# Kernel tuning notes

Measured on AMD Instinct MI355X. Metric: run time of the kernel, lower is better.

The kernel has to match this reference:

```python
import jax, jax.numpy as jnp
import numpy as np

C = 128          # channels (d_model)
D_STATE = 16
D_CONV = 4
EXPAND = 2
D_INNER = EXPAND * C       # 256
DT_RANK = (C + 15) // 16   # 8 (ceil(d_model/16))
B_SZ, H, W = 4, 64, 64


def setup_inputs() -> dict:
    key = jax.random.key(0)
    ks = jax.random.split(key, 12)
    n = lambda k, s, sc=0.02: jax.random.normal(k, s, dtype=jnp.float32) * sc
    return {
        "x": jax.random.normal(ks[0], (B_SZ, C, H, W), dtype=jnp.float32),
        # spatial 3x3 conv
        "conv_spatial_w": n(ks[1], (C, C, 3, 3)),
        "conv_spatial_b": jnp.zeros((C,), jnp.float32),
        # spectral 1x1 conv on [real; imag] concat (2C -> 2C)
        "conv_spectral_w": n(ks[2], (2 * C, 2 * C, 1, 1)),
        "conv_spectral_b": jnp.zeros((2 * C,), jnp.float32),
        # Mamba params (mamba_ssm defaults: in/out_proj no bias, conv1d+dt_proj bias)
        "in_proj_w": n(ks[3], (2 * D_INNER, C)),
        "conv1d_w": n(ks[4], (D_INNER, 1, D_CONV), 0.2),  # depthwise, groups=d_inner
        "conv1d_b": jnp.zeros((D_INNER,), jnp.float32),
        "x_proj_w": n(ks[5], (DT_RANK + 2 * D_STATE, D_INNER)),
        "dt_proj_w": n(ks[6], (D_INNER, DT_RANK), 0.1),
        "dt_proj_b": n(ks[7], (D_INNER,), 0.1),
        "A_log": jnp.log(jnp.broadcast_to(jnp.arange(1, D_STATE + 1, dtype=jnp.float32), (D_INNER, D_STATE))),
        "D": jnp.ones((D_INNER,), jnp.float32),
        "out_proj_w": n(ks[8], (C, D_INNER)),
    }


def _selective_scan(x, dt, A, B, Cm, D):
    # x, dt: [b,l,d]; B, Cm: [b,l,n]; A: [d,n]; D: [d]
    b, l, d = x.shape

    def step(h, inp):
        xt, dtt, Bt, Ct = inp  # [b,d],[b,d],[b,n],[b,n]
        dA = jnp.exp(dtt[..., None] * A)                     # [b,d,n]
        h = dA * h + dtt[..., None] * Bt[:, None, :] * xt[..., None]
        y = jnp.einsum('bdn,bn->bd', h, Ct)
        return h, y

    h0 = jnp.zeros((b, d, A.shape[1]), x.dtype)
    xs = (x.transpose(1, 0, 2), dt.transpose(1, 0, 2),
          B.transpose(1, 0, 2), Cm.transpose(1, 0, 2))
    _, ys = jax.lax.scan(step, h0, xs)
    return ys.transpose(1, 0, 2) + x * D                     # skip term D*x


def _mamba(u, in_proj_w, conv1d_w, conv1d_b, x_proj_w, dt_proj_w, dt_proj_b, A_log, D, out_proj_w):
    # u: [b, l, d_model]
    xz = jnp.einsum('bld,ed->ble', u, in_proj_w)             # [b,l,2*d_inner]
    xi, z = jnp.split(xz, 2, axis=-1)
    # causal depthwise conv1d over sequence
    xc = jax.lax.conv_general_dilated(
        xi.transpose(0, 2, 1), conv1d_w, (1,), ((D_CONV - 1, 0),),
        dimension_numbers=('NCH', 'OIH', 'NCH'), feature_group_count=D_INNER)
    xs = jax.nn.silu((xc + conv1d_b[None, :, None]).transpose(0, 2, 1))  # [b,l,d_inner]
    x_dbl = jnp.einsum('bld,rd->blr', xs, x_proj_w)
    dt = jax.nn.softplus(
        jnp.einsum('blr,dr->bld', x_dbl[..., :DT_RANK], dt_proj_w) + dt_proj_b)
    Bm = x_dbl[..., DT_RANK:DT_RANK + D_STATE]
    Cm = x_dbl[..., DT_RANK + D_STATE:]
    A = -jnp.exp(A_log)
    y = _selective_scan(xs, dt, A, Bm, Cm, D)
    y = y * jax.nn.silu(z)
    return jnp.einsum('bld,od->blo', y, out_proj_w)


def reference(x, conv_spatial_w, conv_spatial_b, conv_spectral_w, conv_spectral_b,
              in_proj_w, conv1d_w, conv1d_b, x_proj_w, dt_proj_w, dt_proj_b,
              A_log, D, out_proj_w):
    b, c, h, w = x.shape
    # spatial branch: 3x3 conv, padding 1
    spatial = jax.lax.conv_general_dilated(
        x, conv_spatial_w, (1, 1), ((1, 1), (1, 1)),
        dimension_numbers=('NCHW', 'OIHW', 'NCHW')) + conv_spatial_b[None, :, None, None]
    # mamba branch over flattened spatial sequence
    u = x.transpose(0, 2, 3, 1).reshape(b, h * w, c)
    ym = _mamba(u, in_proj_w, conv1d_w, conv1d_b, x_proj_w, dt_proj_w, dt_proj_b,
                A_log, D, out_proj_w)
    ym = ym.reshape(b, h, w, c).transpose(0, 3, 1, 2)
    # spectral branch: rfft2 -> concat(real,imag) -> 1x1 conv -> complex -> irfft2
    fft = jnp.fft.rfft2(x, axes=(-2, -1))                    # [b,c,h,w//2+1]
    cat = jnp.concatenate([fft.real, fft.imag], axis=1)      # [b,2c,h,w//2+1]
    fc = jnp.einsum('bchw,oc->bohw', cat, conv_spectral_w[:, :, 0, 0]) \
         + conv_spectral_b[None, :, None, None]
    fr, fi = jnp.split(fc, 2, axis=1)
    spectral = jnp.fft.irfft2(jax.lax.complex(fr, fi), s=(h, w), axes=(-2, -1))
    return spatial + spectral + ym
```

## Files before the change

kernel.cpp:

```cpp
#include <hip/hip_runtime.h>
#include <math.h>

#define PI2 6.283185307179586f
#define SPEC_P 2112
#define NC 64
#define LC 64

typedef __attribute__((ext_vector_type(8))) short s8v;
typedef __attribute__((ext_vector_type(4))) float f4v;
typedef __attribute__((ext_vector_type(4))) unsigned int u4v;
typedef __attribute__((ext_vector_type(4))) unsigned short u16x4;

__device__ __forceinline__ float sigmoidf_(float v){ return 1.0f/(1.0f+__expf(-v)); }
__device__ __forceinline__ float siluf_(float v){ return v*sigmoidf_(v); }
__device__ __forceinline__ float softplusf_(float v){ return fmaxf(v,0.0f)+log1pf(__expf(-fabsf(v))); }
__device__ __forceinline__ float bf2f(ushort u){ union{unsigned u; float f;} x; x.u=((unsigned)u)<<16; return x.f; }
__device__ __forceinline__ ushort f2bf(float f){ union{float f; unsigned u;} x; x.f=f; return (ushort)((x.u + 0x7FFFu + ((x.u>>16)&1u))>>16); }
__device__ __forceinline__ float u2f_hi(unsigned w){ union{unsigned u; float f;} x; x.u = w & 0xffff0000u; return x.f; }
__device__ __forceinline__ float u2f_lo(unsigned w){ union{unsigned u; float f;} x; x.u = w << 16; return x.f; }

__global__ void __launch_bounds__(256) k_prep_all(
        const float* __restrict__ x, const float* __restrict__ csw,
        const float* __restrict__ dtw, const float* __restrict__ xpw,
        const float* __restrict__ ipw, const float* __restrict__ opw,
        const float* __restrict__ spw, const float* __restrict__ c1w,
        ushort* __restrict__ xT, ushort* __restrict__ wsp, ushort* __restrict__ cxw,
        ushort* __restrict__ ipwb, ushort* __restrict__ opwb, ushort* __restrict__ spwb,
        ushort* __restrict__ gE1, ushort* __restrict__ gE2f,
        ushort* __restrict__ gE2i, ushort* __restrict__ gE3,
        float* __restrict__ cwT){
    __shared__ float ld[128][65];
    int tid=threadIdx.x;
    if(blockIdx.x < 256){
        int bh=blockIdx.x; int b=bh>>6, h=bh&63;
        for(int i=tid;i<8192;i+=256){ int c=i>>6, w=i&63;
            ld[c][w] = x[((size_t)((b<<7)+c)<<12) + (h<<6) + w]; }
        __syncthreads();
        for(int i=tid;i<8192;i+=256){ int w=i>>7, c=i&127;
            xT[((size_t)bh<<13) + (w<<7) + c] = f2bf(ld[c][w]); }
        return;
    }
    int i = (blockIdx.x-256)*256+tid;
    if(i<147456){
        int p = i>>14; int rem = i&16383; int o=rem>>7, c=rem&127;
        wsp[i] = f2bf(csw[(size_t)(o*128+c)*9 + p]);
    } else if(i<212992){
        int j = i-147456; int e=j>>8, c=j&255;
        float s=0.f;
        #pragma unroll
        for(int r=0;r<8;r++) s += dtw[e*8+r]*xpw[r*256+c];
        cxw[j]=f2bf(s);
    } else if(i<221184){
        int t=i-212992; cxw[65536+t]=f2bf(xpw[2048+t]);
    } else if(i<286720){
        int t=i-221184; ipwb[t]=f2bf(ipw[t]);
    } else if(i<319488){
        int t=i-286720; opwb[t]=f2bf(opw[t]);
    } else if(i<385024){
        int t=i-319488; spwb[t]=f2bf(spw[t]);
    } else if(i<389248){
        int j=i-385024; int r=j>>6, w=j&63; float v;
        if(r<33){ int t=(w*r)&63; v = cosf(PI2*(float)t/64.0f); }
        else    { int t=(w*(r-33))&63; v = -sinf(PI2*(float)t/64.0f); }
        gE1[j]=f2bf(v);
    } else if(i<405632){
        int j=i-389248; int col=j>>7, k=j&127; int h=k&63, rk=k>>6, kh=col&63, rc=col>>6;
        int t=(h*kh)&63; float cv=cosf(PI2*(float)t/64.0f), sv=sinf(PI2*(float)t/64.0f);
        float v = (rc==0) ? (rk==0? cv : sv) : (rk==0? -sv : cv);
        gE2f[j]=f2bf(v);
    } else if(i<422016){
        int j=i-405632; int col=j>>7, k=j&127; int h=col&63, rc=col>>6, kh=k&63, rk=k>>6;
        int t=(h*kh)&63; float cv=cosf(PI2*(float)t/64.0f), sv=sinf(PI2*(float)t/64.0f);
        float v = (rc==0) ? (rk==0? cv : -sv) : (rk==0? sv : cv);
        gE2i[j]=f2bf(v);
    } else if(i<428160){
        int j=i-422016; int w=j/96, k=j-w*96; float v=0.f;
        if(k<33){
            int kw=k;
            if(kw==0) v=1.f;
            else if(kw==32) v=(w&1)? -1.f : 1.f;
            else { int t=(kw*w)&63; v=2.f*cosf(PI2*(float)t/64.0f); }
        } else if(k<66){
            int kw=k-33;
            if(kw==0||kw==32) v=0.f;
            else { int t=(kw*w)&63; v=-2.f*sinf(PI2*(float)t/64.0f); }
        }
        gE3[j]=f2bf(v);
    } else if(i<429184){
        int j=i-428160; int k=j>>8, d=j&255;
        cwT[j] = c1w[d*4+k];
    }
}

template<int BM,int BN,int WR,int WC,int BK,int KT>
__device__ __forceinline__ void gemm_body(const ushort* __restrict__ Ag, int lda,
                                          const ushort* __restrict__ Bg, int ldb,
                                          int m0, int n0, f4v* acc, ushort* smem){
    constexpr int MR = BM/(WR*16);
    constexpr int NR = BN/(WC*16);
    constexpr int AW = BK+8;
    ushort (*As)[AW] = (ushort(*)[AW])smem;
    ushort (*Bs)[AW] = (ushort(*)[AW])(smem + BM*AW);
    const int tid=threadIdx.x, lane=tid&63, wid=tid>>6;
    const int l15=lane&15, lhi=lane>>4;
    const int wr=wid/WC, wc=wid%WC;
    for(int kb=0;kb<KT;kb++){
        __syncthreads();
        for(int v=tid; v<BM*(BK/8); v+=256){ int r=v/(BK/8), cv=(v%(BK/8))*8;
            *(s8v*)&As[r][cv] = *(const s8v*)&Ag[(size_t)(m0+r)*lda + kb*BK + cv]; }
        for(int v=tid; v<BN*(BK/8); v+=256){ int r=v/(BK/8), cv=(v%(BK/8))*8;
            *(s8v*)&Bs[r][cv] = *(const s8v*)&Bg[(size_t)(n0+r)*ldb + kb*BK + cv]; }
        __syncthreads();
        #pragma unroll
        for(int ck=0;ck<BK/32;ck++){
            s8v a[MR], bb[NR];
            #pragma unroll
            for(int i=0;i<MR;i++) a[i] = *(const s8v*)&As[wr*(BM/WR)+i*16+l15][ck*32+lhi*8];
            #pragma unroll
            for(int j=0;j<NR;j++) bb[j] = *(const s8v*)&Bs[wc*(BN/WC)+j*16+l15][ck*32+lhi*8];
            #pragma unroll
            for(int i=0;i<MR;i++)
                #pragma unroll
                for(int j=0;j<NR;j++)
                    acc[i*NR+j] = __builtin_amdgcn_mfma_f32_16x16x32_bf16(a[i], bb[j], acc[i*NR+j],0,0,0);
        }
    }
}

__device__ __forceinline__ void body_spatial(int bx, const ushort* __restrict__ xT,
        const ushort* __restrict__ wsp, const float* __restrict__ csb,
        float* __restrict__ out, ushort* smem){
    ushort (*slab)[66][72] = (ushort(*)[66][72])smem;
    int bh = bx>>1, oh = bx&1;
    int b = bh>>6, h = bh&63;
    int tid = threadIdx.x, lane = tid&63, wid = tid>>6;
    int l15 = lane&15, lhi = lane>>4;
    s8v zv = {0,0,0,0,0,0,0,0};
    if(tid < 48){
        int khp = tid>>4; int rem = tid&15;
        int row = (rem>>3)*65, cv = (rem&7)*8;
        *(s8v*)&slab[khp][row][cv] = zv;
    }
    f4v acc[4];
    f4v zf = {0.f,0.f,0.f,0.f};
    #pragma unroll
    for(int j=0;j<4;j++) acc[j]=zf;
    int orow = oh*64 + wid*16 + l15;
    for(int kb=0;kb<2;kb++){
        __syncthreads();
        for(int khh=0;khh<3;khh++){
            int hh = h-1+khh;
            if(hh>=0 && hh<64){
                const ushort* src = xT + (((size_t)(b<<6)+hh)<<13) + kb*64;
                for(int v=tid; v<512; v+=256){
                    int w = v>>3, cv = (v&7)*8;
                    *(s8v*)&slab[khh][w+1][cv] = *(const s8v*)&src[(w<<7)+cv];
                }
            } else {
                for(int v=tid; v<512; v+=256){
                    int w = v>>3, cv = (v&7)*8;
                    *(s8v*)&slab[khh][w+1][cv] = zv;
                }
            }
        }
        __syncthreads();
        for(int p=0;p<9;p++){
            int khh = p/3, kw = p - khh*3;
            const ushort* wrow = wsp + (size_t)p*16384 + (orow<<7) + kb*64;
            #pragma unroll
            for(int ck=0;ck<2;ck++){
                s8v a = *(const s8v*)&wrow[ck*32+lhi*8];
                #pragma unroll
                for(int j=0;j<4;j++){
                    s8v bf = *(const s8v*)&slab[khh][j*16+l15+kw][ck*32+lhi*8];
                    acc[j] = __builtin_amdgcn_mfma_f32_16x16x32_bf16(a, bf, acc[j],0,0,0);
                }
            }
        }
    }
    #pragma unroll
    for(int r=0;r<4;r++){
        int o = oh*64 + wid*16 + lhi*4 + r;
        float bv = csb[o];
        size_t rowbase = (((size_t)(b<<7)+o)<<12) + (h<<6);
        #pragma unroll
        for(int j=0;j<4;j++){
            out[rowbase + j*16 + l15] = acc[j][r] + bv;
        }
    }
}

__device__ __forceinline__ void body_inproj(int j, const ushort* __restrict__ xT,
        const ushort* __restrict__ ipw, ushort* __restrict__ xi, ushort* __restrict__ z,
        ushort* smem){
    int m0 = (j&127)*128, n0 = (j>>7)*128;
    f4v acc[16];
    f4v zf = {0.f,0.f,0.f,0.f};
    #pragma unroll
    for(int q=0;q<16;q++) acc[q]=zf;
    gemm_body<128,128,2,2,64,2>(xT,128, ipw,128, m0,n0, acc, smem);
    int tid=threadIdx.x, lane=tid&63, wid=tid>>6, l15=lane&15, lhi=lane>>4;
    int wr=wid>>1, wc=wid&1;
    #pragma unroll
    for(int i=0;i<4;i++)
        #pragma unroll
        for(int jj=0;jj<4;jj++)
            #pragma unroll
            for(int r=0;r<4;r++){
                int m = m0 + wr*64 + i*16 + lhi*4 + r;
                int e = n0 + wc*64 + jj*16 + l15;
                ushort v = f2bf(acc[i*4+jj][r]);
                if(e<256) xi[(size_t)m*256+e]=v; else z[(size_t)m*256+e-256]=v;
            }
}

__device__ __forceinline__ void body_spec_fwd(int bc, const float* __restrict__ x,
        const ushort* __restrict__ gE1, const ushort* __restrict__ gE2f,
        ushort* __restrict__ rit, ushort* smem){
    ushort (*Xs)[72]  = (ushort(*)[72])smem;
    ushort (*E1s)[72] = (ushort(*)[72])(smem+4608);
    ushort (*T2s)[136]= (ushort(*)[136])(smem+10368);
    ushort (*EB)[72]  = (ushort(*)[72])smem;
    int b = bc>>7, c = bc&127;
    int tid=threadIdx.x, lane=tid&63, wid=tid>>6, l15=lane&15, lhi=lane>>4;
    const float* xsrc = x + ((size_t)bc<<12);
    for(int v=tid; v<1024; v+=256){
        int h=v>>4, w0=(v&15)<<2;
        float4 f = *(const float4*)&xsrc[(h<<6)+w0];
        Xs[h][w0]=f2bf(f.x); Xs[h][w0+1]=f2bf(f.y); Xs[h][w0+2]=f2bf(f.z); Xs[h][w0+3]=f2bf(f.w);
    }
    for(int v=tid; v<528; v+=256){ int r=v>>3, k0=(v&7)<<3;
        *(s8v*)&E1s[r][k0] = *(const s8v*)&gE1[(r<<6)+k0]; }
    __syncthreads();
    {
        f4v accA[5];
        f4v zf={0.f,0.f,0.f,0.f};
        #pragma unroll
        for(int j=0;j<5;j++) accA[j]=zf;
        int m0 = wid<<4;
        #pragma unroll
        for(int ck=0;ck<2;ck++){
            s8v a = *(const s8v*)&Xs[m0+l15][ck*32+lhi*8];
            #pragma unroll
            for(int j=0;j<5;j++){
                s8v bb = *(const s8v*)&E1s[j*16+l15][ck*32+lhi*8];
                accA[j] = __builtin_amdgcn_mfma_f32_16x16x32_bf16(a, bb, accA[j],0,0,0);
            }
        }
        #pragma unroll
        for(int j=0;j<5;j++){
            int c_ = j*16+l15;
            #pragma unroll
            for(int r=0;r<4;r++){
                int h = m0 + lhi*4 + r;
                if(c_ < 33)      T2s[c_][h]       = f2bf(accA[j][r]);
                else if(c_ < 66) T2s[c_-33][64+h] = f2bf(accA[j][r]);
            }
        }
    }
    f4v accB[6];
    {
        f4v zf={0.f,0.f,0.f,0.f};
        #pragma unroll
        for(int q=0;q<6;q++) accB[q]=zf;
    }
    for(int kb=0;kb<2;kb++){
        __syncthreads();
        for(int v=tid; v<1024; v+=256){ int r=v>>3, k0=(v&7)<<3;
            *(s8v*)&EB[r][k0] = *(const s8v*)&gE2f[(r<<7) + kb*64 + k0]; }
        __syncthreads();
        #pragma unroll
        for(int rt=0; rt<3; rt++){
            #pragma unroll
            for(int ck=0;ck<2;ck++){
                s8v a  = *(const s8v*)&T2s[rt*16+l15][kb*64 + ck*32+lhi*8];
                s8v b0 = *(const s8v*)&EB[(wid*2)*16+l15][ck*32+lhi*8];
                s8v b1 = *(const s8v*)&EB[(wid*2+1)*16+l15][ck*32+lhi*8];
                accB[rt*2+0] = __builtin_amdgcn_mfma_f32_16x16x32_bf16(a, b0, accB[rt*2+0],0,0,0);
                accB[rt*2+1] = __builtin_amdgcn_mfma_f32_16x16x32_bf16(a, b1, accB[rt*2+1],0,0,0);
            }
        }
    }
    #pragma unroll
    for(int rt=0; rt<3; rt++){
        int col0 = wid*32 + l15;
        int col1 = wid*32 + 16 + l15;
        int kh0 = col0&63, ri0 = col0>>6;
        int kh1 = col1&63, ri1 = col1>>6;
        #pragma unroll
        for(int r=0;r<4;r++){
            int kw = rt*16 + lhi*4 + r;
            if(kw<33){
                rit[((size_t)(b*2112) + kh0*33 + kw)*256 + ri0*128 + c] = f2bf(accB[rt*2+0][r]);
                rit[((size_t)(b*2112) + kh1*33 + kw)*256 + ri1*128 + c] = f2bf(accB[rt*2+1][r]);
            }
        }
    }
}

__global__ void __launch_bounds__(256) k_stage1(
        const float* __restrict__ x, const ushort* __restrict__ xT,
        const ushort* __restrict__ wsp, const float* __restrict__ csb,
        const ushort* __restrict__ ipwb, const ushort* __restrict__ gE1,
        const ushort* __restrict__ gE2f,
        float* __restrict__ out, ushort* __restrict__ xi, ushort* __restrict__ zb,
        ushort* __restrict__ rit){
    __shared__ __align__(16) ushort smem[18432];
    int bx = blockIdx.x;
    if(bx < 512)       body_spatial(bx, xT, wsp, csb, out, smem);
    else if(bx < 1024) body_inproj(bx-512, xT, ipwb, xi, zb, smem);
    else               body_spec_fwd(bx-1024, x, gE1, gE2f, rit, smem);
}

__device__ __forceinline__ void body_conv1d(int blk, const ushort* __restrict__ xi,
        const float* __restrict__ cwT, const float* __restrict__ cb, ushort* __restrict__ xs){
    int flat = blk*256 + threadIdx.x;
    int d8 = (flat & 31) << 3;
    int bl = flat >> 5;
    int l  = bl & 4095;
    s8v zv = {0,0,0,0,0,0,0,0};
    s8v x0 = *(const s8v*)&xi[(size_t)bl*256 + d8];
    s8v x1 = (l>=1)? *(const s8v*)&xi[(size_t)(bl-1)*256 + d8] : zv;
    s8v x2 = (l>=2)? *(const s8v*)&xi[(size_t)(bl-2)*256 + d8] : zv;
    s8v x3 = (l>=3)? *(const s8v*)&xi[(size_t)(bl-3)*256 + d8] : zv;
    f4v w0a = *(const f4v*)&cwT[0*256+d8], w0b = *(const f4v*)&cwT[0*256+d8+4];
    f4v w1a = *(const f4v*)&cwT[1*256+d8], w1b = *(const f4v*)&cwT[1*256+d8+4];
    f4v w2a = *(const f4v*)&cwT[2*256+d8], w2b = *(const f4v*)&cwT[2*256+d8+4];
    f4v w3a = *(const f4v*)&cwT[3*256+d8], w3b = *(const f4v*)&cwT[3*256+d8+4];
    f4v ba  = *(const f4v*)&cb[d8], bbv = *(const f4v*)&cb[d8+4];
    s8v outv;
    #pragma unroll
    for(int j=0;j<8;j++){
        float w0 = (j<4)? w0a[j] : w0b[j-4];
        float w1 = (j<4)? w1a[j] : w1b[j-4];
        float w2 = (j<4)? w2a[j] : w2b[j-4];
        float w3 = (j<4)? w3a[j] : w3b[j-4];
        float bs = (j<4)? ba[j]  : bbv[j-4];
        float acc = bs + bf2f((ushort)x3[j])*w0 + bf2f((ushort)x2[j])*w1
                       + bf2f((ushort)x1[j])*w2 + bf2f((ushort)x0[j])*w3;
        outv[j] = (short)f2bf(siluf_(acc));
    }
    *(s8v*)&xs[(size_t)bl*256 + d8] = outv;
}

__global__ void __launch_bounds__(256) k_stage2(
        const ushort* __restrict__ xi, const float* __restrict__ cwT,
        const float* __restrict__ c1b, ushort* __restrict__ xs,
        const ushort* __restrict__ rit, const ushort* __restrict__ spwb,
        const float* __restrict__ spb, ushort* __restrict__ Frb, ushort* __restrict__ Fib){
    __shared__ __align__(16) ushort smem[13824];
    int bx = blockIdx.x;
    if(bx < 2048){ body_conv1d(bx, xi, cwT, c1b, xs); return; }
    int jj = bx - 2048;
    int nt = jj/132, mt = jj - nt*132;
    int m0 = mt*64, n0 = nt*128;
    f4v acc[8];
    f4v zf = {0.f,0.f,0.f,0.f};
    #pragma unroll
    for(int q=0;q<8;q++) acc[q]=zf;
    gemm_body<64,128,2,2,64,4>(rit,256, spwb,256, m0,n0, acc, smem);
    int tid=threadIdx.x, lane=tid&63, wid=tid>>6, l15=lane&15, lhi=lane>>4;
    int wr=wid>>1, wc=wid&1;
    #pragma unroll
    for(int i=0;i<2;i++)
        #pragma unroll
        for(int j=0;j<4;j++){
            int m = m0 + wr*32 + i*16 + lhi*4;
            int bb = m/SPEC_P, p = m - bb*SPEC_P;
            int e = n0 + wc*64 + j*16 + l15;
            f4v v = acc[i*4+j] + spb[e];
            u16x4 pk;
            pk.x=f2bf(v[0]); pk.y=f2bf(v[1]); pk.z=f2bf(v[2]); pk.w=f2bf(v[3]);
            ushort* dst = (e<128)? &Frb[((size_t)(bb*128+e))*SPEC_P+p]
                                 : &Fib[((size_t)(bb*128+e-128))*SPEC_P+p];
            *(u16x4*)dst = pk;
        }
}

__device__ __forceinline__ void body_xdbl(int j, const ushort* __restrict__ xs,
        const ushort* __restrict__ cxw, const float* __restrict__ dtb,
        ushort* __restrict__ dtBC, ushort* smem){
    int m0 = (j&127)*128, n0 = (j>>7)*96;
    f4v acc[12];
    f4v zf = {0.f,0.f,0.f,0.f};
    #pragma unroll
    for(int q=0;q<12;q++) acc[q]=zf;
// ... 24 lines not shown
    const ushort* fr = Frb + (size_t)bo*SPEC_P;
    const ushort* fi = Fib + (size_t)bo*SPEC_P;
    for(int p=tid; p<2112; p+=256){
        int kh = p/33, kw = p - kh*33;
        A1s[kw][kh]    = fr[p];
        A1s[kw][64+kh] = fi[p];
    }
    f4v accB[6];
    {
        f4v zf={0.f,0.f,0.f,0.f};
        #pragma unroll
        for(int q=0;q<6;q++) accB[q]=zf;
    }
    for(int kb=0;kb<2;kb++){
        __syncthreads();
        for(int v=tid; v<1024; v+=256){ int r=v>>3, k0=(v&7)<<3;
            *(s8v*)&EB[r][k0] = *(const s8v*)&gE2i[(r<<7) + kb*64 + k0]; }
        __syncthreads();
        #pragma unroll
        for(int rt=0; rt<3; rt++){
            #pragma unroll
            for(int ck=0;ck<2;ck++){
                s8v a  = *(const s8v*)&A1s[rt*16+l15][kb*64 + ck*32+lhi*8];
                s8v b0 = *(const s8v*)&EB[(wid*2)*16+l15][ck*32+lhi*8];
                s8v b1 = *(const s8v*)&EB[(wid*2+1)*16+l15][ck*32+lhi*8];
                accB[rt*2+0] = __builtin_amdgcn_mfma_f32_16x16x32_bf16(a, b0, accB[rt*2+0],0,0,0);
                accB[rt*2+1] = __builtin_amdgcn_mfma_f32_16x16x32_bf16(a, b1, accB[rt*2+1],0,0,0);
            }
        }
    }
    __syncthreads();
    {
        s8v zvv = {0,0,0,0,0,0,0,0};
        for(int v=tid; v<256; v+=256){}
        if(tid<256){ int r=tid>>2, c0=64+((tid&3)<<3); *(s8v*)&T3s[r][c0]=zvv; }
    }
    for(int v=tid; v<768; v+=256){ int r=v/12, k0=(v-r*12)*8;
        *(s8v*)&E3s[r][k0] = *(const s8v*)&gE3[r*96+k0]; }
    __syncthreads();
    #pragma unroll
    for(int rt=0; rt<3; rt++){
        int col0 = wid*32 + l15;
        int col1 = wid*32 + 16 + l15;
        int h0 = col0&63, ri0 = col0>>6;
        int h1 = col1&63, ri1 = col1>>6;
        #pragma unroll
        for(int r=0;r<4;r++){
            int kw = rt*16 + lhi*4 + r;
            if(kw<33){
                T3s[h0][ri0? 33+kw : kw] = f2bf(accB[rt*2+0][r]);
                T3s[h1][ri1? 33+kw : kw] = f2bf(accB[rt*2+1][r]);
            }
        }
    }
    __syncthreads();
    {
        int m0 = wid<<4;
        f4v acc[4];
        f4v zf={0.f,0.f,0.f,0.f};
        #pragma unroll
        for(int j=0;j<4;j++) acc[j]=zf;
        #pragma unroll
        for(int ck=0;ck<3;ck++){
            s8v a = *(const s8v*)&T3s[m0+l15][ck*32+lhi*8];
            #pragma unroll
            for(int j=0;j<4;j++){
                s8v bb = *(const s8v*)&E3s[j*16+l15][ck*32+lhi*8];
                acc[j] = __builtin_amdgcn_mfma_f32_16x16x32_bf16(a, bb, acc[j],0,0,0);
            }
        }
        ushort* obase = specT + ((size_t)bo<<12);
        #pragma unroll
        for(int j=0;j<4;j++){
            int w = j*16+l15;
            #pragma unroll
            for(int r=0;r<4;r++){
                int h = m0 + lhi*4 + r;
                obase[(h<<6)+w] = f2bf(acc[j][r]*(1.0f/4096.0f));
            }
        }
    }
}

__global__ void __launch_bounds__(256) k_stage3(
        const ushort* __restrict__ xs, const ushort* __restrict__ cxw,
        const float* __restrict__ dtb, ushort* __restrict__ dtBC,
        const ushort* __restrict__ Frb, const ushort* __restrict__ Fib,
        const ushort* __restrict__ gE2i, const ushort* __restrict__ gE3,
        ushort* __restrict__ specT){
    __shared__ __align__(16) ushort smem[16128];
    int bx = blockIdx.x;
    if(bx < 384) body_xdbl(bx, xs, cxw, dtb, dtBC, smem);
    else         body_spec_inv(bx-384, Frb, Fib, gE2i, gE3, specT, smem);
}

__global__ void __launch_bounds__(256) k_scan(
        const ushort* __restrict__ xs, const ushort* __restrict__ dtBC,
        const ushort* __restrict__ z, const float* __restrict__ A_log,
        const float* __restrict__ Dp, ushort* __restrict__ ys){
    __shared__ unsigned sdx[LC*16];
    __shared__ unsigned sbc[LC*16];
    __shared__ ushort   sz[LC*16];
    __shared__ float    sY[16*272];
    int blk = blockIdx.x;
    int c   = blk & (NC-1);
    int bdg = blk >> 6;
    int b = bdg >> 4, dg = bdg & 15;
    int d_base = dg*16;
    int tid = threadIdx.x;
    int g = tid>>4, n = tid&15;
    int d = d_base + g;
    float An = -__expf(A_log[d*16+n]);
    float DdR = Dp[d_base + n];
    {
        int lc = tid>>2, part = tid&3;
        size_t r = (size_t)(b*4096 + c*64 + lc);
        if(part<2){
// ... 32 lines not shown
    for(int t4=0;t4<4;t4++){
        #pragma unroll
        for(int k=0;k<16;k++){
            int lc = t4*16+k;
            unsigned wdx = pdx[lc*16];
            unsigned wbc = pbc[lc*16];
            float dtv = u2f_lo(wdx);
            float xv  = u2f_hi(wdx);
            float Bv  = u2f_lo(wbc);
            float Cv  = u2f_hi(wbc);
            float dA  = __expf(dtv*An);
            h = dA*h + (dtv*xv)*Bv;
            psy[k*272] = h*Cv;
        }
        __syncthreads();
        {
            float s = 0.f;
            const float* pr = &sY[tt*272 + g2];
            #pragma unroll
            for(int n2=0;n2<16;n2++) s += pr[n2*17];
            int lcg = t4*16+tt;
            float xv2 = u2f_hi(sdx[lcg*16+g2]);
            float zv  = bf2f(sz[lcg*16+g2]);
            float yv  = (s + xv2*DdR) * siluf_(zv);
            ys[(size_t)(b*4096 + c*64 + lcg)*256 + d_base + g2] = f2bf(yv);
        }
        __syncthreads();
    }
}

__global__ void __launch_bounds__(256) k_final(const ushort* __restrict__ ys,
                                               const ushort* __restrict__ opw,
                                               const ushort* __restrict__ specT,
                                               float* __restrict__ out){
    __shared__ __align__(16) ushort smem[13824];
    int m0 = blockIdx.x*64;
    f4v acc[8];
    f4v zf = {0.f,0.f,0.f,0.f};
    #pragma unroll
    for(int q=0;q<8;q++) acc[q]=zf;
    gemm_body<64,128,2,2,64,4>(ys,256, opw,256, m0,0, acc, smem);
    int tid=threadIdx.x, lane=tid&63, wid=tid>>6, l15=lane&15, lhi=lane>>4;
    int wr=wid>>1, wc=wid&1;
    #pragma unroll
    for(int i=0;i<2;i++)
        #pragma unroll
        for(int j=0;j<4;j++){
            int m = m0 + wr*32 + i*16 + lhi*4;
            int o = wc*64 + j*16 + l15;
            int bb = m>>12, l = m&4095;
            size_t oidx = (((size_t)(bb<<7)+o)<<12)+l;
            f4v old = *(f4v*)&out[oidx];
            u16x4 sp = *(const u16x4*)&specT[oidx];
            f4v spv = {bf2f(sp.x), bf2f(sp.y), bf2f(sp.z), bf2f(sp.w)};
            *(f4v*)&out[oidx] = old + acc[i*4+j] + spv;
        }
}

extern "C" void kernel_launch(void* const* d_in, const int* in_sizes, int n_in,
                              void* d_out, int out_size, void* d_ws, size_t ws_size,
                              hipStream_t stream){
    const float* x    = (const float*)d_in[0];
    const float* csw  = (const float*)d_in[1];
    const float* csb  = (const float*)d_in[2];
    const float* spw  = (const float*)d_in[3];
    const float* spb  = (const float*)d_in[4];
    const float* ipw  = (const float*)d_in[5];
    const float* c1w  = (const float*)d_in[6];
    const float* c1b  = (const float*)d_in[7];
    const float* xpw  = (const float*)d_in[8];
    const float* dtw  = (const float*)d_in[9];
    const float* dtb  = (const float*)d_in[10];
    const float* alog = (const float*)d_in[11];
    const float* Dp   = (const float*)d_in[12];
    const float* opw  = (const float*)d_in[13];
    float* out = (float*)d_out;

    ushort* uw   = (ushort*)d_ws;
    ushort* xT   = uw;
    ushort* wsp  = xT + 2097152;
    ushort* ipwb = wsp + 147456;
    ushort* cxw  = ipwb + 65536;
    ushort* opwb = cxw + 73728;
    ushort* spwb = opwb + 32768;
    ushort* gE1  = spwb + 65536;
    ushort* gE2f = gE1 + 4352;
    ushort* gE2i = gE2f + 16384;
    ushort* gE3  = gE2i + 16384;
    ushort* xi   = gE3 + 6144;
    ushort* zb   = xi + 4194304;
    ushort* xs   = zb + 4194304;
    ushort* dtBC = xs + 4194304;
    ushort* Frb  = dtBC + 4718592;
    ushort* Fib  = Frb + 2162688;
    ushort* rit  = Fib + 2162688;
    float*  cwT  = (float*)(rit + 2162688);
    ushort* specT = rit;

    k_prep_all<<<1933,256,0,stream>>>(x, csw, dtw, xpw, ipw, opw, spw, c1w,
                                      xT, wsp, cxw, ipwb, opwb, spwb,
                                      gE1, gE2f, gE2i, gE3, cwT);
    k_stage1<<<1536,256,0,stream>>>(x, xT, wsp, csb, ipwb, gE1, gE2f,
                                    out, xi, zb, rit);
    k_stage2<<<2312,256,0,stream>>>(xi, cwT, c1b, xs, rit, spwb, spb, Frb, Fib);
    k_stage3<<<896,256,0,stream>>>(xs, cxw, dtb, dtBC, Frb, Fib, gE2i, gE3, specT);
    k_scan<<<4096,256,0,stream>>>(xs, dtBC, zb, alog, Dp, xi );
    k_final<<<256,256,0,stream>>>(xi , opwb, specT, out);
}
```

Baseline: 136.4 us.

## Restructure pipeline: fuse conv1d into in-proj, move spectral forward into prep kernel

The spectral forward DFT now runs inside the first (prep) kernel, with twiddles generated in shared memory rather than loaded from global tables. The in-projection is split into an x-half that applies the causal depthwise conv1d and SiLU in its epilogue using a 16-row halo, and a separate z-half. That removes the standalone conv1d pass and the round trip of xi through memory. The spatial conv output goes to a bf16 buffer summed in the final kernel, so the read-modify-write of out is gone at some precision cost. The final GEMM tile is halved to launch more blocks, and the halo rows recompute extra in-projection work.

Measured after the change: 141.3 us. +3.6%, slower.

```diff
diff --git a/kernel.cpp b/kernel.cpp
--- a/kernel.cpp
+++ b/kernel.cpp
@@ -18,79 +18,6 @@
 __device__ __forceinline__ ushort f2bf(float f){ union{float f; unsigned u;} x; x.f=f; return (ushort)((x.u + 0x7FFFu + ((x.u>>16)&1u))>>16); }
 __device__ __forceinline__ float u2f_hi(unsigned w){ union{unsigned u; float f;} x; x.u = w & 0xffff0000u; return x.f; }
 __device__ __forceinline__ float u2f_lo(unsigned w){ union{unsigned u; float f;} x; x.u = w << 16; return x.f; }
-
-__global__ void __launch_bounds__(256) k_prep_all(
-        const float* __restrict__ x, const float* __restrict__ csw,
-        const float* __restrict__ dtw, const float* __restrict__ xpw,
-        const float* __restrict__ ipw, const float* __restrict__ opw,
-        const float* __restrict__ spw, const float* __restrict__ c1w,
-        ushort* __restrict__ xT, ushort* __restrict__ wsp, ushort* __restrict__ cxw,
-        ushort* __restrict__ ipwb, ushort* __restrict__ opwb, ushort* __restrict__ spwb,
-        ushort* __restrict__ gE1, ushort* __restrict__ gE2f,
-        ushort* __restrict__ gE2i, ushort* __restrict__ gE3,
-        float* __restrict__ cwT){
-    __shared__ float ld[128][65];
-    int tid=threadIdx.x;
-    if(blockIdx.x < 256){
-        int bh=blockIdx.x; int b=bh>>6, h=bh&63;
-        for(int i=tid;i<8192;i+=256){ int c=i>>6, w=i&63;
-            ld[c][w] = x[((size_t)((b<<7)+c)<<12) + (h<<6) + w]; }
-        __syncthreads();
-        for(int i=tid;i<8192;i+=256){ int w=i>>7, c=i&127;
-            xT[((size_t)bh<<13) + (w<<7) + c] = f2bf(ld[c][w]); }
-        return;
-    }
-    int i = (blockIdx.x-256)*256+tid;
-    if(i<147456){
-        int p = i>>14; int rem = i&16383; int o=rem>>7, c=rem&127;
-        wsp[i] = f2bf(csw[(size_t)(o*128+c)*9 + p]);
-    } else if(i<212992){
-        int j = i-147456; int e=j>>8, c=j&255;
-        float s=0.f;
-        #pragma unroll
-        for(int r=0;r<8;r++) s += dtw[e*8+r]*xpw[r*256+c];
-        cxw[j]=f2bf(s);
-    } else if(i<221184){
-        int t=i-212992; cxw[65536+t]=f2bf(xpw[2048+t]);
-    } else if(i<286720){
-        int t=i-221184; ipwb[t]=f2bf(ipw[t]);
-    } else if(i<319488){
-        int t=i-286720; opwb[t]=f2bf(opw[t]);
-    } else if(i<385024){
-        int t=i-319488; spwb[t]=f2bf(spw[t]);
-    } else if(i<389248){
-        int j=i-385024; int r=j>>6, w=j&63; float v;
-        if(r<33){ int t=(w*r)&63; v = cosf(PI2*(float)t/64.0f); }
-        else    { int t=(w*(r-33))&63; v = -sinf(PI2*(float)t/64.0f); }
-        gE1[j]=f2bf(v);
-    } else if(i<405632){
-        int j=i-389248; int col=j>>7, k=j&127; int h=k&63, rk=k>>6, kh=col&63, rc=col>>6;
-        int t=(h*kh)&63; float cv=cosf(PI2*(float)t/64.0f), sv=sinf(PI2*(float)t/64.0f);
-        float v = (rc==0) ? (rk==0? cv : sv) : (rk==0? -sv : cv);
-        gE2f[j]=f2bf(v);
-    } else if(i<422016){
-        int j=i-405632; int col=j>>7, k=j&127; int h=col&63, rc=col>>6, kh=k&63, rk=k>>6;
-        int t=(h*kh)&63; float cv=cosf(PI2*(float)t/64.0f), sv=sinf(PI2*(float)t/64.0f);
-        float v = (rc==0) ? (rk==0? cv : -sv) : (rk==0? sv : cv);
-        gE2i[j]=f2bf(v);
-    } else if(i<428160){
-        int j=i-422016; int w=j/96, k=j-w*96; float v=0.f;
-        if(k<33){
-            int kw=k;
-            if(kw==0) v=1.f;
-            else if(kw==32) v=(w&1)? -1.f : 1.f;
-            else { int t=(kw*w)&63; v=2.f*cosf(PI2*(float)t/64.0f); }
-        } else if(k<66){
-            int kw=k-33;
-            if(kw==0||kw==32) v=0.f;
-            else { int t=(kw*w)&63; v=-2.f*sinf(PI2*(float)t/64.0f); }
-        }
-        gE3[j]=f2bf(v);
-    } else if(i<429184){
-        int j=i-428160; int k=j>>8, d=j&255;
-        cwT[j] = c1w[d*4+k];
-    }
-}
 
 template<int BM,int BN,int WR,int WC,int BK,int KT>
 __device__ __forceinline__ void gemm_body(const ushort* __restrict__ Ag, int lda,
@@ -127,9 +54,166 @@
     }
 }
 
+__device__ __forceinline__ void body_spec_fwd(int bc, const float* __restrict__ x,
+        ushort* __restrict__ rit, ushort* smem){
+    ushort (*Xs)[72]  = (ushort(*)[72])smem;
+    ushort (*E1s)[72] = (ushort(*)[72])(smem+4608);
+    ushort (*T2s)[136]= (ushort(*)[136])(smem+10368);
+    ushort (*EB)[72]  = (ushort(*)[72])smem;
+    float* cs = (float*)(smem+16896);
+    float* sn = cs + 64;
+    int b = bc>>7, c = bc&127;
+    int tid=threadIdx.x, lane=tid&63, wid=tid>>6, l15=lane&15, lhi=lane>>4;
+    if(tid<64){ float s,co; sincosf(PI2*(float)tid/64.0f,&s,&co); cs[tid]=co; sn[tid]=s; }
+    const float* xsrc = x + ((size_t)bc<<12);
+    for(int v=tid; v<1024; v+=256){
+        int h=v>>4, w0=(v&15)<<2;
+        float4 f = *(const float4*)&xsrc[(h<<6)+w0];
+        Xs[h][w0]=f2bf(f.x); Xs[h][w0+1]=f2bf(f.y); Xs[h][w0+2]=f2bf(f.z); Xs[h][w0+3]=f2bf(f.w);
+    }
+    __syncthreads();
+    for(int v=tid; v<5120; v+=256){ int r=v>>6, w=v&63; float val=0.f;
+        if(r<33) val = cs[(w*r)&63];
+        else if(r<66) val = -sn[(w*(r-33))&63];
+        E1s[r][w] = f2bf(val); }
+    __syncthreads();
+    {
+        f4v accA[5];
+        f4v zf={0.f,0.f,0.f,0.f};
+        #pragma unroll
+        for(int j=0;j<5;j++) accA[j]=zf;
+        int m0 = wid<<4;
+        #pragma unroll
+        for(int ck=0;ck<2;ck++){
+            s8v a = *(const s8v*)&Xs[m0+l15][ck*32+lhi*8];
+            #pragma unroll
+            for(int j=0;j<5;j++){
+                s8v bb = *(const s8v*)&E1s[j*16+l15][ck*32+lhi*8];
+                accA[j] = __builtin_amdgcn_mfma_f32_16x16x32_bf16(a, bb, accA[j],0,0,0);
+            }
+        }
+        #pragma unroll
+        for(int j=0;j<5;j++){
+            int c_ = j*16+l15;
+            #pragma unroll
+            for(int r=0;r<4;r++){
+                int h = m0 + lhi*4 + r;
+                if(c_ < 33)      T2s[c_][h]       = f2bf(accA[j][r]);
+                else if(c_ < 66) T2s[c_-33][64+h] = f2bf(accA[j][r]);
+            }
+        }
+    }
+    f4v accB[6];
+    {
+        f4v zf={0.f,0.f,0.f,0.f};
+        #pragma unroll
+        for(int q=0;q<6;q++) accB[q]=zf;
+    }
+    for(int kb=0;kb<2;kb++){
+        __syncthreads();
+        for(int v=tid; v<8192; v+=256){ int r=v>>6, k=v&63; int kk=kb*64+k;
+            int hh=kk&63, rk=kk>>6, kh=r&63, rc=r>>6;
+            int t=(hh*kh)&63;
+            float val = (rc==0) ? (rk==0? cs[t] : sn[t]) : (rk==0? -sn[t] : cs[t]);
+            EB[r][k]=f2bf(val); }
+        __syncthreads();
+        #pragma unroll
+        for(int rt=0; rt<3; rt++){
+            #pragma unroll
+            for(int ck=0;ck<2;ck++){
+                s8v a  = *(const s8v*)&T2s[rt*16+l15][kb*64 + ck*32+lhi*8];
+                s8v b0 = *(const s8v*)&EB[(wid*2)*16+l15][ck*32+lhi*8];
+                s8v b1 = *(const s8v*)&EB[(wid*2+1)*16+l15][ck*32+lhi*8];
+                accB[rt*2+0] = __builtin_amdgcn_mfma_f32_16x16x32_bf16(a, b0, accB[rt*2+0],0,0,0);
+                accB[rt*2+1] = __builtin_amdgcn_mfma_f32_16x16x32_bf16(a, b1, accB[rt*2+1],0,0,0);
+            }
+        }
+    }
+    #pragma unroll
+    for(int rt=0; rt<3; rt++){
+        int col0 = wid*32 + l15;
+        int col1 = wid*32 + 16 + l15;
+        int kh0 = col0&63, ri0 = col0>>6;
+        int kh1 = col1&63, ri1 = col1>>6;
+        #pragma unroll
+        for(int r=0;r<4;r++){
+            int kw = rt*16 + lhi*4 + r;
+            if(kw<33){
+                rit[((size_t)(b*2112) + kh0*33 + kw)*256 + ri0*128 + c] = f2bf(accB[rt*2+0][r]);
+                rit[((size_t)(b*2112) + kh1*33 + kw)*256 + ri1*128 + c] = f2bf(accB[rt*2+1][r]);
+            }
+        }
+    }
+}
+
+__global__ void __launch_bounds__(256) k_d1(
+        const float* __restrict__ x, const float* __restrict__ csw,
+        const float* __restrict__ dtw, const float* __restrict__ xpw,
+        const float* __restrict__ ipw, const float* __restrict__ opw,
+        const float* __restrict__ spw, const float* __restrict__ c1w,
+        ushort* __restrict__ xT, ushort* __restrict__ wsp, ushort* __restrict__ cxw,
+        ushort* __restrict__ ipwb, ushort* __restrict__ opwb, ushort* __restrict__ spwb,
+        ushort* __restrict__ gE2i, ushort* __restrict__ gE3,
+        float* __restrict__ cwT, ushort* __restrict__ rit){
+    __shared__ __align__(16) ushort smem[17152];
+    int tid=threadIdx.x;
+    int bx=blockIdx.x;
+    if(bx < 256){
+        float (*ld)[65] = (float(*)[65])smem;
+        int bh=bx; int b=bh>>6, h=bh&63;
+        for(int i=tid;i<8192;i+=256){ int c=i>>6, w=i&63;
+            ld[c][w] = x[((size_t)((b<<7)+c)<<12) + (h<<6) + w]; }
+        __syncthreads();
+        for(int i=tid;i<8192;i+=256){ int w=i>>7, c=i&127;
+            xT[((size_t)bh<<13) + (w<<7) + c] = f2bf(ld[c][w]); }
+        return;
+    }
+    if(bx >= 1933){ body_spec_fwd(bx-1933, x, rit, smem); return; }
+    int i = (bx-256)*256+tid;
+    if(i<147456){
+        int p = i>>14; int rem = i&16383; int o=rem>>7, c=rem&127;
+        wsp[i] = f2bf(csw[(size_t)(o*128+c)*9 + p]);
+    } else if(i<212992){
+        int j = i-147456; int e=j>>8, c=j&255;
+        float s=0.f;
+        #pragma unroll
+        for(int r=0;r<8;r++) s += dtw[e*8+r]*xpw[r*256+c];
+        cxw[j]=f2bf(s);
+    } else if(i<221184){
+        int t=i-212992; cxw[65536+t]=f2bf(xpw[2048+t]);
+    } else if(i<286720){
+        int t=i-221184; ipwb[t]=f2bf(ipw[t]);
+    } else if(i<319488){
+        int t=i-286720; opwb[t]=f2bf(opw[t]);
+    } else if(i<385024){
+        int t=i-319488; spwb[t]=f2bf(spw[t]);
+    } else if(i<401408){
+        int j=i-385024; int col=j>>7, k=j&127; int h=col&63, rc=col>>6, kh=k&63, rk=k>>6;
+        int t=(h*kh)&63; float cv=cosf(PI2*(float)t/64.0f), sv=sinf(PI2*(float)t/64.0f);
+        float v = (rc==0) ? (rk==0? cv : -sv) : (rk==0? sv : cv);
+        gE2i[j]=f2bf(v);
+    } else if(i<407552){
+        int j=i-401408; int w=j/96, k=j-w*96; float v=0.f;
+        if(k<33){
+            int kw=k;
+            if(kw==0) v=1.f;
+            else if(kw==32) v=(w&1)? -1.f : 1.f;
+            else { int t=(kw*w)&63; v=2.f*cosf(PI2*(float)t/64.0f); }
+        } else if(k<66){
+            int kw=k-33;
+            if(kw==0||kw==32) v=0.f;
+            else { int t=(kw*w)&63; v=-2.f*sinf(PI2*(float)t/64.0f); }
+        }
+        gE3[j]=f2bf(v);
+    } else if(i<408576){
+        int j=i-407552; int k=j>>8, d=j&255;
+        cwT[j] = c1w[d*4+k];
+    }
+}
+
 __device__ __forceinline__ void body_spatial(int bx, const ushort* __restrict__ xT,
         const ushort* __restrict__ wsp, const float* __restrict__ csb,
-        float* __restrict__ out, ushort* smem){
+        ushort* __restrict__ spatT, ushort* smem){
     ushort (*slab)[66][72] = (ushort(*)[66][72])smem;
     int bh = bx>>1, oh = bx&1;
     int b = bh>>6, h = bh&63;
@@ -185,15 +269,79 @@
         size_t rowbase = (((size_t)(b<<7)+o)<<12) + (h<<6);
         #pragma unroll
         for(int j=0;j<4;j++){
-            out[rowbase + j*16 + l15] = acc[j][r] + bv;
-        }
-    }
-}
-
-__device__ __forceinline__ void body_inproj(int j, const ushort* __restrict__ xT,
-        const ushort* __restrict__ ipw, ushort* __restrict__ xi, ushort* __restrict__ z,
-        ushort* smem){
-    int m0 = (j&127)*128, n0 = (j>>7)*128;
+            spatT[rowbase + j*16 + l15] = f2bf(acc[j][r] + bv);
+        }
+    }
+}
+
+__device__ __forceinline__ void body_inprojA(int j, const ushort* __restrict__ xT,
+        const ushort* __restrict__ ipw, const float* __restrict__ cwT,
+        const float* __restrict__ c1b, ushort* __restrict__ xs, ushort* smem){
+    int m0=(j&127)*128, n0=(j>>7)*128;
+    int l0 = m0 & 4095;
+    ushort (*As)[72]=(ushort(*)[72])smem;
+    ushort (*Bs)[72]=(ushort(*)[72])(smem+10368);
+    ushort (*xiL)[132]=(ushort(*)[132])smem;
+    int tid=threadIdx.x, lane=tid&63, wid=tid>>6, l15=lane&15, lhi=lane>>4;
+    s8v zv = {0,0,0,0,0,0,0,0};
+    f4v acc[18];
+    {
+        f4v zf={0.f,0.f,0.f,0.f};
+        #pragma unroll
+        for(int q=0;q<18;q++) acc[q]=zf;
+    }
+    for(int kb=0;kb<2;kb++){
+        __syncthreads();
+        for(int v=tid; v<1152; v+=256){ int r=v>>3, cv=(v&7)*8;
+            s8v val = zv;
+            if(r>=16 || l0!=0){
+                int gm = m0-16+r;
+                val = *(const s8v*)&xT[(size_t)gm*128 + kb*64 + cv];
+            }
+            *(s8v*)&As[r][cv]=val; }
+        for(int v=tid; v<1024; v+=256){ int r=v>>3, cv=(v&7)*8;
+            *(s8v*)&Bs[r][cv] = *(const s8v*)&ipw[(size_t)(n0+r)*128 + kb*64+cv]; }
+        __syncthreads();
+        #pragma unroll
+        for(int ck=0;ck<2;ck++){
+            s8v a[9], bb[2];
+            #pragma unroll
+            for(int i=0;i<9;i++) a[i] = *(const s8v*)&As[i*16+l15][ck*32+lhi*8];
+            #pragma unroll
+            for(int jj=0;jj<2;jj++) bb[jj] = *(const s8v*)&Bs[wid*32+jj*16+l15][ck*32+lhi*8];
+            #pragma unroll
+            for(int i=0;i<9;i++)
+                #pragma unroll
+                for(int jj=0;jj<2;jj++)
+                    acc[i*2+jj] = __builtin_amdgcn_mfma_f32_16x16x32_bf16(a[i], bb[jj], acc[i*2+jj],0,0,0);
+        }
+    }
+    __syncthreads();
+    #pragma unroll
+    for(int i=0;i<9;i++)
+        #pragma unroll
+        for(int jj=0;jj<2;jj++)
+            #pragma unroll
+            for(int r=0;r<4;r++)
+                xiL[i*16+lhi*4+r][wid*32+jj*16+l15] = f2bf(acc[i*2+jj][r]);
+    __syncthreads();
+    int ct = tid&127, half=tid>>7;
+    int e = n0+ct;
+    float w0=cwT[0*256+e], w1=cwT[1*256+e], w2=cwT[2*256+e], w3=cwT[3*256+e];
+    float bs=c1b[e];
+    int rbase = 16 + half*64;
+    float t0=bf2f(xiL[rbase-3][ct]), t1=bf2f(xiL[rbase-2][ct]), t2=bf2f(xiL[rbase-1][ct]);
+    for(int i=0;i<64;i++){
+        float t3=bf2f(xiL[rbase+i][ct]);
+        float a = bs + t0*w0+t1*w1+t2*w2+t3*w3;
+        xs[(size_t)(m0+half*64+i)*256 + e] = f2bf(siluf_(a));
+        t0=t1; t1=t2; t2=t3;
+    }
+}
+
+__device__ __forceinline__ void body_inprojZ(int j, const ushort* __restrict__ xT,
+        const ushort* __restrict__ ipw, ushort* __restrict__ z, ushort* smem){
+    int m0 = (j&127)*128, n0 = 256+(j>>7)*128;
     f4v acc[16];
     f4v zf = {0.f,0.f,0.f,0.f};
     #pragma unroll
@@ -209,149 +357,23 @@
             for(int r=0;r<4;r++){
                 int m = m0 + wr*64 + i*16 + lhi*4 + r;
                 int e = n0 + wc*64 + jj*16 + l15;
-                ushort v = f2bf(acc[i*4+jj][r]);
-                if(e<256) xi[(size_t)m*256+e]=v; else z[(size_t)m*256+e-256]=v;
-            }
-}
-
-__device__ __forceinline__ void body_spec_fwd(int bc, const float* __restrict__ x,
-        const ushort* __restrict__ gE1, const ushort* __restrict__ gE2f,
-        ushort* __restrict__ rit, ushort* smem){
-    ushort (*Xs)[72]  = (ushort(*)[72])smem;
-    ushort (*E1s)[72] = (ushort(*)[72])(smem+4608);
-    ushort (*T2s)[136]= (ushort(*)[136])(smem+10368);
-    ushort (*EB)[72]  = (ushort(*)[72])smem;
-    int b = bc>>7, c = bc&127;
-    int tid=threadIdx.x, lane=tid&63, wid=tid>>6, l15=lane&15, lhi=lane>>4;
-    const float* xsrc = x + ((size_t)bc<<12);
-    for(int v=tid; v<1024; v+=256){
-        int h=v>>4, w0=(v&15)<<2;
-        float4 f = *(const float4*)&xsrc[(h<<6)+w0];
-        Xs[h][w0]=f2bf(f.x); Xs[h][w0+1]=f2bf(f.y); Xs[h][w0+2]=f2bf(f.z); Xs[h][w0+3]=f2bf(f.w);
-    }
-    for(int v=tid; v<528; v+=256){ int r=v>>3, k0=(v&7)<<3;
-        *(s8v*)&E1s[r][k0] = *(const s8v*)&gE1[(r<<6)+k0]; }
-    __syncthreads();
-    {
-        f4v accA[5];
-        f4v zf={0.f,0.f,0.f,0.f};
-        #pragma unroll
-        for(int j=0;j<5;j++) accA[j]=zf;
-        int m0 = wid<<4;
-        #pragma unroll
-        for(int ck=0;ck<2;ck++){
-            s8v a = *(const s8v*)&Xs[m0+l15][ck*32+lhi*8];
-            #pragma unroll
-            for(int j=0;j<5;j++){
-                s8v bb = *(const s8v*)&E1s[j*16+l15][ck*32+lhi*8];
-                accA[j] = __builtin_amdgcn_mfma_f32_16x16x32_bf16(a, bb, accA[j],0,0,0);
-            }
-        }
-        #pragma unroll
-        for(int j=0;j<5;j++){
-            int c_ = j*16+l15;
-            #pragma unroll
-            for(int r=0;r<4;r++){
-                int h = m0 + lhi*4 + r;
-                if(c_ < 33)      T2s[c_][h]       = f2bf(accA[j][r]);
-                else if(c_ < 66) T2s[c_-33][64+h] = f2bf(accA[j][r]);
-            }
-        }
-    }
-    f4v accB[6];
-    {
-        f4v zf={0.f,0.f,0.f,0.f};
-        #pragma unroll
-        for(int q=0;q<6;q++) accB[q]=zf;
-    }
-    for(int kb=0;kb<2;kb++){
-        __syncthreads();
-        for(int v=tid; v<1024; v+=256){ int r=v>>3, k0=(v&7)<<3;
-            *(s8v*)&EB[r][k0] = *(const s8v*)&gE2f[(r<<7) + kb*64 + k0]; }
-        __syncthreads();
-        #pragma unroll
-        for(int rt=0; rt<3; rt++){
-            #pragma unroll
-            for(int ck=0;ck<2;ck++){
-                s8v a  = *(const s8v*)&T2s[rt*16+l15][kb*64 + ck*32+lhi*8];
-                s8v b0 = *(const s8v*)&EB[(wid*2)*16+l15][ck*32+lhi*8];
-                s8v b1 = *(const s8v*)&EB[(wid*2+1)*16+l15][ck*32+lhi*8];
-                accB[rt*2+0] = __builtin_amdgcn_mfma_f32_16x16x32_bf16(a, b0, accB[rt*2+0],0,0,0);
-                accB[rt*2+1] = __builtin_amdgcn_mfma_f32_16x16x32_bf16(a, b1, accB[rt*2+1],0,0,0);
-            }
-        }
-    }
-    #pragma unroll
-    for(int rt=0; rt<3; rt++){
-        int col0 = wid*32 + l15;
-        int col1 = wid*32 + 16 + l15;
-        int kh0 = col0&63, ri0 = col0>>6;
-        int kh1 = col1&63, ri1 = col1>>6;
-        #pragma unroll
-        for(int r=0;r<4;r++){
-            int kw = rt*16 + lhi*4 + r;
-            if(kw<33){
-                rit[((size_t)(b*2112) + kh0*33 + kw)*256 + ri0*128 + c] = f2bf(accB[rt*2+0][r]);
-                rit[((size_t)(b*2112) + kh1*33 + kw)*256 + ri1*128 + c] = f2bf(accB[rt*2+1][r]);
-            }
-        }
-    }
-}
-
-__global__ void __launch_bounds__(256) k_stage1(
-        const float* __restrict__ x, const ushort* __restrict__ xT,
-        const ushort* __restrict__ wsp, const float* __restrict__ csb,
-        const ushort* __restrict__ ipwb, const ushort* __restrict__ gE1,
-        const ushort* __restrict__ gE2f,
-        float* __restrict__ out, ushort* __restrict__ xi, ushort* __restrict__ zb,
-        ushort* __restrict__ rit){
-    __shared__ __align__(16) ushort smem[18432];
-    int bx = blockIdx.x;
-    if(bx < 512)       body_spatial(bx, xT, wsp, csb, out, smem);
-    else if(bx < 1024) body_inproj(bx-512, xT, ipwb, xi, zb, smem);
-    else               body_spec_fwd(bx-1024, x, gE1, gE2f, rit, smem);
-}
-
-__device__ __forceinline__ void body_conv1d(int blk, const ushort* __restrict__ xi,
-        const float* __restrict__ cwT, const float* __restrict__ cb, ushort* __restrict__ xs){
-    int flat = blk*256 + threadIdx.x;
-    int d8 = (flat & 31) << 3;
-    int bl = flat >> 5;
-    int l  = bl & 4095;
-    s8v zv = {0,0,0,0,0,0,0,0};
-    s8v x0 = *(const s8v*)&xi[(size_t)bl*256 + d8];
-    s8v x1 = (l>=1)? *(const s8v*)&xi[(size_t)(bl-1)*256 + d8] : zv;
-    s8v x2 = (l>=2)? *(const s8v*)&xi[(size_t)(bl-2)*256 + d8] : zv;
-    s8v x3 = (l>=3)? *(const s8v*)&xi[(size_t)(bl-3)*256 + d8] : zv;
-    f4v w0a = *(const f4v*)&cwT[0*256+d8], w0b = *(const f4v*)&cwT[0*256+d8+4];
-    f4v w1a = *(const f4v*)&cwT[1*256+d8], w1b = *(const f4v*)&cwT[1*256+d8+4];
-    f4v w2a = *(const f4v*)&cwT[2*256+d8], w2b = *(const f4v*)&cwT[2*256+d8+4];
-    f4v w3a = *(const f4v*)&cwT[3*256+d8], w3b = *(const f4v*)&cwT[3*256+d8+4];
-    f4v ba  = *(const f4v*)&cb[d8], bbv = *(const f4v*)&cb[d8+4];
-    s8v outv;
-    #pragma unroll
-    for(int j=0;j<8;j++){
-        float w0 = (j<4)? w0a[j] : w0b[j-4];
-        float w1 = (j<4)? w1a[j] : w1b[j-4];
-        float w2 = (j<4)? w2a[j] : w2b[j-4];
-        float w3 = (j<4)? w3a[j] : w3b[j-4];
-        float bs = (j<4)? ba[j]  : bbv[j-4];
-        float acc = bs + bf2f((ushort)x3[j])*w0 + bf2f((ushort)x2[j])*w1
-                       + bf2f((ushort)x1[j])*w2 + bf2f((ushort)x0[j])*w3;
-        outv[j] = (short)f2bf(siluf_(acc));
-    }
-    *(s8v*)&xs[(size_t)bl*256 + d8] = outv;
-}
-
-__global__ void __launch_bounds__(256) k_stage2(
-        const ushort* __restrict__ xi, const float* __restrict__ cwT,
-        const float* __restrict__ c1b, ushort* __restrict__ xs,
+                z[(size_t)m*256 + (e-256)] = f2bf(acc[i*4+jj][r]);
+            }
+}
+
+__global__ void __launch_bounds__(256) k_d2(
+        const ushort* __restrict__ xT, const ushort* __restrict__ wsp,
+        const float* __restrict__ csb, ushort* __restrict__ spatT,
+        const ushort* __restrict__ ipwb, const float* __restrict__ cwT,
+        const float* __restrict__ c1b, ushort* __restrict__ xs, ushort* __restrict__ zb,
         const ushort* __restrict__ rit, const ushort* __restrict__ spwb,
         const float* __restrict__ spb, ushort* __restrict__ Frb, ushort* __restrict__ Fib){
-    __shared__ __align__(16) ushort smem[13824];
+    __shared__ __align__(16) ushort smem[19584];
     int bx = blockIdx.x;
-    if(bx < 2048){ body_conv1d(bx, xi, cwT, c1b, xs); return; }
-    int jj = bx - 2048;
+    if(bx < 512){ body_spatial(bx, xT, wsp, csb, spatT, smem); return; }
+    if(bx < 768){ body_inprojA(bx-512, xT, ipwb, cwT, c1b, xs, smem); return; }
+    if(bx < 1024){ body_inprojZ(bx-768, xT, ipwb, zb, smem); return; }
+    int jj = bx - 1024;
     int nt = jj/132, mt = jj - nt*132;
     int m0 = mt*64, n0 = nt*128;
     f4v acc[8];
@@ -442,8 +464,8 @@
     __syncthreads();
     {
         s8v zvv = {0,0,0,0,0,0,0,0};
-        for(int v=tid; v<256; v+=256){}
-        if(tid<256){ int r=tid>>2, c0=64+((tid&3)<<3); *(s8v*)&T3s[r][c0]=zvv; }
+        int r=tid>>2, c0=64+((tid&3)<<3);
+        *(s8v*)&T3s[r][c0]=zvv;
     }
     for(int v=tid; v<768; v+=256){ int r=v/12, k0=(v-r*12)*8;
         *(s8v*)&E3s[r][k0] = *(const s8v*)&gE3[r*96+k0]; }
@@ -492,7 +514,7 @@
     }
 }
 
-__global__ void __launch_bounds__(256) k_stage3(
+__global__ void __launch_bounds__(256) k_d3(
         const ushort* __restrict__ xs, const ushort* __restrict__ cxw,
         const float* __restrict__ dtb, ushort* __restrict__ dtBC,
         const ushort* __restrict__ Frb, const ushort* __restrict__ Fib,
@@ -591,29 +613,32 @@
 __global__ void __launch_bounds__(256) k_final(const ushort* __restrict__ ys,
                                                const ushort* __restrict__ opw,
                                                const ushort* __restrict__ specT,
+                                               const ushort* __restrict__ spatT,
                                                float* __restrict__ out){
-    __shared__ __align__(16) ushort smem[13824];
-    int m0 = blockIdx.x*64;
-    f4v acc[8];
+    __shared__ __align__(16) ushort smem[11520];
+    int m0 = blockIdx.x*32;
+    f4v acc[4];
     f4v zf = {0.f,0.f,0.f,0.f};
     #pragma unroll
-    for(int q=0;q<8;q++) acc[q]=zf;
-    gemm_body<64,128,2,2,64,4>(ys,256, opw,256, m0,0, acc, smem);
+    for(int q=0;q<4;q++) acc[q]=zf;
+    gemm_body<32,128,2,2,64,4>(ys,256, opw,256, m0,0, acc, smem);
     int tid=threadIdx.x, lane=tid&63, wid=tid>>6, l15=lane&15, lhi=lane>>4;
     int wr=wid>>1, wc=wid&1;
     #pragma unroll
-    for(int i=0;i<2;i++)
-        #pragma unroll
-        for(int j=0;j<4;j++){
-            int m = m0 + wr*32 + i*16 + lhi*4;
-            int o = wc*64 + j*16 + l15;
-            int bb = m>>12, l = m&4095;
-            size_t oidx = (((size_t)(bb<<7)+o)<<12)+l;
-            f4v old = *(f4v*)&out[oidx];
-            u16x4 sp = *(const u16x4*)&specT[oidx];
-            f4v spv = {bf2f(sp.x), bf2f(sp.y), bf2f(sp.z), bf2f(sp.w)};
-            *(f4v*)&out[oidx] = old + acc[i*4+j] + spv;
-        }
+    for(int j=0;j<4;j++){
+        int m = m0 + wr*16 + lhi*4;
+        int o = wc*64 + j*16 + l15;
+        int bb = m>>12, l = m&4095;
+        size_t oidx = (((size_t)(bb<<7)+o)<<12)+l;
+        u16x4 sp = *(const u16x4*)&specT[oidx];
+        u16x4 st = *(const u16x4*)&spatT[oidx];
+        f4v v;
+        v[0] = acc[j][0] + bf2f(sp.x) + bf2f(st.x);
+        v[1] = acc[j][1] + bf2f(sp.y) + bf2f(st.y);
+        v[2] = acc[j][2] + bf2f(sp.z) + bf2f(st.z);
+        v[3] = acc[j][3] + bf2f(sp.w) + bf2f(st.w);
+        *(f4v*)&out[oidx] = v;
+    }
 }
 
 extern "C" void kernel_launch(void* const* d_in, const int* in_sizes, int n_in,
@@ -642,27 +667,25 @@
     ushort* cxw  = ipwb + 65536;
     ushort* opwb = cxw + 73728;
     ushort* spwb = opwb + 32768;
-    ushort* gE1  = spwb + 65536;
-    ushort* gE2f = gE1 + 4352;
-    ushort* gE2i = gE2f + 16384;
+    ushort* gE2i = spwb + 65536;
     ushort* gE3  = gE2i + 16384;
-    ushort* xi   = gE3 + 6144;
-    ushort* zb   = xi + 4194304;
+    ushort* ys   = gE3 + 6144;
+    ushort* zb   = ys + 4194304;
     ushort* xs   = zb + 4194304;
     ushort* dtBC = xs + 4194304;
     ushort* Frb  = dtBC + 4718592;
     ushort* Fib  = Frb + 2162688;
     ushort* rit  = Fib + 2162688;
-    float*  cwT  = (float*)(rit + 2162688);
+    ushort* spatT= rit + 2162688;
+    float*  cwT  = (float*)(spatT + 2097152);
     ushort* specT = rit;
 
-    k_prep_all<<<1933,256,0,stream>>>(x, csw, dtw, xpw, ipw, opw, spw, c1w,
-                                      xT, wsp, cxw, ipwb, opwb, spwb,
-                                      gE1, gE2f, gE2i, gE3, cwT);
-    k_stage1<<<1536,256,0,stream>>>(x, xT, wsp, csb, ipwb, gE1, gE2f,
-                                    out, xi, zb, rit);
-    k_stage2<<<2312,256,0,stream>>>(xi, cwT, c1b, xs, rit, spwb, spb, Frb, Fib);
-    k_stage3<<<896,256,0,stream>>>(xs, cxw, dtb, dtBC, Frb, Fib, gE2i, gE3, specT);
-    k_scan<<<4096,256,0,stream>>>(xs, dtBC, zb, alog, Dp, xi );
-    k_final<<<256,256,0,stream>>>(xi , opwb, specT, out);
-}
+    k_d1<<<2445,256,0,stream>>>(x, csw, dtw, xpw, ipw, opw, spw, c1w,
+                                xT, wsp, cxw, ipwb, opwb, spwb,
+                                gE2i, gE3, cwT, rit);
+    k_d2<<<1288,256,0,stream>>>(xT, wsp, csb, spatT, ipwb, cwT, c1b,
+                                xs, zb, rit, spwb, spb, Frb, Fib);
+    k_d3<<<896,256,0,stream>>>(xs, cxw, dtb, dtBC, Frb, Fib, gE2i, gE3, specT);
+    k_scan<<<4096,256,0,stream>>>(xs, dtBC, zb, alog, Dp, ys);
+    k_final<<<512,256,0,stream>>>(ys, opwb, specT, spatT, out);
+}
```
